# Kernel tuning notes

Hardware: AMD Instinct MI355X
Metric: run time of the kernel (lower is better)

## Reference

```python
import jax, jax.numpy as jnp
import numpy as np

N_USERS = 100_000
N_ENTITIES = 200_000
N_EDGES = 1_000_000
NNZ = 1_000_000
C = 64          # embedding dim
N_FACTORS = 4
N_REL_M1 = 10   # n_relations - 1
N_HOPS = 2
TEMP = 0.2


def setup_inputs() -> dict:
    key = jax.random.key(0)
    ks = jax.random.split(key, 10)
    return {
        'user_emb': jax.random.normal(ks[0], (N_USERS, C), jnp.float32) * 0.1,
        'entity_emb': jax.random.normal(ks[1], (N_ENTITIES, C), jnp.float32) * 0.1,
        'latent_emb': jax.random.normal(ks[2], (N_FACTORS, C), jnp.float32) * 0.1,
        'weight': jax.random.normal(ks[3], (N_REL_M1, C), jnp.float32) * 0.1,
        'disen_weight_att': jax.random.normal(ks[4], (N_FACTORS, N_REL_M1), jnp.float32) * 0.1,
        'edge_index': jax.random.randint(ks[5], (2, N_EDGES), 0, N_ENTITIES, dtype=jnp.int32),
        'edge_type': jax.random.randint(ks[6], (N_EDGES,), 1, N_REL_M1 + 1, dtype=jnp.int32),
        'inter_rows': jax.random.randint(ks[7], (NNZ,), 0, N_USERS, dtype=jnp.int32),
        'inter_cols': jax.random.randint(ks[8], (NNZ,), 0, N_ENTITIES, dtype=jnp.int32),
        'inter_vals': jax.random.uniform(ks[9], (NNZ,), jnp.float32),
    }


def _l2norm(x):
    # F.normalize(x, dim=1) with eps=1e-12
    n = jnp.linalg.norm(x, axis=1, keepdims=True)
    return x / jnp.maximum(n, 1e-12)


def _mutual_information(disen_weight_att):
    disen_T = disen_weight_att.T                                    # [R-1, F]
    nd = disen_T / jnp.linalg.norm(disen_T, axis=1, keepdims=True)
    pos_scores = jnp.sum(nd * nd, axis=1)
    ttl_scores = jnp.sum(disen_T @ disen_weight_att, axis=1)
    pos = jnp.exp(pos_scores / TEMP)
    ttl = jnp.exp(ttl_scores / TEMP)
    return -jnp.sum(jnp.log(pos / ttl))


def reference(user_emb, entity_emb, latent_emb, weight, disen_weight_att,
              edge_index, edge_type, inter_rows, inter_cols, inter_vals):
    entity_res = entity_emb
    user_res = user_emb
    cor = _mutual_information(disen_weight_att)

    head, tail = edge_index[0], edge_index[1]
    # edge degree for scatter_mean (constant across hops)
    cnt = jax.ops.segment_sum(jnp.ones((N_EDGES,), jnp.float32), head,
                              num_segments=N_ENTITIES)
    inv_cnt = 1.0 / jnp.maximum(cnt, 1.0)

    for _ in range(N_HOPS):
        # KG aggregate: gather tail entities, modulate by relation, scatter-mean to head
        rel = weight[edge_type - 1]                                  # [E, C]
        neigh = entity_emb[tail] * rel                               # [E, C]
        entity_agg = jax.ops.segment_sum(neigh, head, num_segments=N_ENTITIES)
        entity_agg = entity_agg * inv_cnt[:, None]

        # user -> latent factor attention
        score = jax.nn.softmax(user_emb @ latent_emb.T, axis=1)[:, :, None]  # [U, F, 1]

        # sparse user aggregate: interact_mat @ entity_emb
        user_agg = jax.ops.segment_sum(inter_vals[:, None] * entity_emb[inter_cols],
                                       inter_rows, num_segments=N_USERS)     # [U, C]

        disen_weight = jax.nn.softmax(disen_weight_att, axis=-1) @ weight    # [F, C]
        user_agg = user_agg * jnp.sum(disen_weight[None] * score, axis=1) + user_agg

        entity_emb = _l2norm(entity_agg)
        user_emb = _l2norm(user_agg)
        entity_res = entity_res + entity_emb
        user_res = user_res + user_emb

    return entity_res, user_res, cor
```

## Files before the change

### kernel.cpp

```cpp
#include <hip/hip_runtime.h>
#include <math.h>

#define N_USERS    100000
#define N_ENTITIES 200000
#define N_EDGES    1000000
#define NNZ        1000000
#define CDIM       64
#define N_FACTORS  4
#define N_REL      10
#define TEMP       0.2f

#define CB         1024
#define NBE        196
#define NBU        98
#define ACHUNK     4096
#define GA         245
#define GCVT       6250
#define KG_BLOCKS  6250
#define USER_BLOCKS 3125
#define PCHUNK     4096
#define GPE        49
#define GPU_       25

typedef unsigned int u32;
typedef unsigned short u16;
typedef unsigned char u8;

#if defined(__has_builtin)
#if __has_builtin(__builtin_amdgcn_cvt_pk_f32_fp8) && __has_builtin(__builtin_amdgcn_cvt_pk_fp8_f32)
#define HAVE_HW_FP8 1
#endif
#endif

__device__ __forceinline__ float bflo(u32 w) { return __uint_as_float(w << 16); }
__device__ __forceinline__ float bfhi(u32 w) { return __uint_as_float(w & 0xFFFF0000u); }
__device__ __forceinline__ u16 f2bf(float f) {
    u32 u = __float_as_uint(f);
    u32 r = u + 0x7FFFu + ((u >> 16) & 1u);
    return (u16)(r >> 16);
}
__device__ __forceinline__ void unpack8_bf(uint4 rv, float* x) {
    x[0] = bflo(rv.x); x[1] = bfhi(rv.x);
    x[2] = bflo(rv.y); x[3] = bfhi(rv.y);
    x[4] = bflo(rv.z); x[5] = bfhi(rv.z);
    x[6] = bflo(rv.w); x[7] = bfhi(rv.w);
}
__device__ __forceinline__ uint4 pack8_bf(const float* x) {
    uint4 o;
    o.x = (u32)f2bf(x[0]) | ((u32)f2bf(x[1]) << 16);
    o.y = (u32)f2bf(x[2]) | ((u32)f2bf(x[3]) << 16);
    o.z = (u32)f2bf(x[4]) | ((u32)f2bf(x[5]) << 16);
    o.w = (u32)f2bf(x[6]) | ((u32)f2bf(x[7]) << 16);
    return o;
}

#ifndef HAVE_HW_FP8
__device__ __forceinline__ float fp8_dec1(u32 b) {
    u32 s = b >> 7, em = b & 0x7F;
    float mag;
    if (em < 8) mag = (float)em * 0.001953125f;
    else {
        u32 bits = (((em >> 3) + 120u) << 23) | ((em & 7u) << 20);
        mag = __uint_as_float(bits);
    }
    return s ? -mag : mag;
}
__device__ __forceinline__ u32 fp8_enc1(float f) {
    float a = fabsf(f);
    u32 s = (__float_as_uint(f) >> 31) << 7;
    if (a < 0.015625f) {
        int n = (int)rintf(a * 512.0f);
        return s | (u32)n;
    }
    u32 u = __float_as_uint(a);
    u32 r = u + 0x0007FFFFu + ((u >> 20) & 1u);
    int ee = (int)((r >> 23) & 0xFF) - 127 + 7;
    if (ee >= 16) return s | 0x7Eu;
    return s | ((u32)ee << 3) | ((r >> 20) & 7u);
}
#endif

__device__ __forceinline__ void unpack8_fp8(uint2 rv, float* x) {
#ifdef HAVE_HW_FP8
    typedef float floatx2 __attribute__((ext_vector_type(2)));
    floatx2 a0 = __builtin_amdgcn_cvt_pk_f32_fp8(rv.x, false);
    floatx2 a1 = __builtin_amdgcn_cvt_pk_f32_fp8(rv.x, true);
    floatx2 a2 = __builtin_amdgcn_cvt_pk_f32_fp8(rv.y, false);
    floatx2 a3 = __builtin_amdgcn_cvt_pk_f32_fp8(rv.y, true);
    x[0] = a0.x; x[1] = a0.y; x[2] = a1.x; x[3] = a1.y;
    x[4] = a2.x; x[5] = a2.y; x[6] = a3.x; x[7] = a3.y;
#else
    x[0] = fp8_dec1(rv.x & 0xFF);         x[1] = fp8_dec1((rv.x >> 8) & 0xFF);
    x[2] = fp8_dec1((rv.x >> 16) & 0xFF); x[3] = fp8_dec1(rv.x >> 24);
    x[4] = fp8_dec1(rv.y & 0xFF);         x[5] = fp8_dec1((rv.y >> 8) & 0xFF);
    x[6] = fp8_dec1((rv.y >> 16) & 0xFF); x[7] = fp8_dec1(rv.y >> 24);
#endif
}
__device__ __forceinline__ uint2 pack8_fp8(const float* x) {
    uint2 o;
#ifdef HAVE_HW_FP8
    int v0 = 0, v1 = 0;
    v0 = __builtin_amdgcn_cvt_pk_fp8_f32(x[0], x[1], v0, false);
    v0 = __builtin_amdgcn_cvt_pk_fp8_f32(x[2], x[3], v0, true);
    v1 = __builtin_amdgcn_cvt_pk_fp8_f32(x[4], x[5], v1, false);
    v1 = __builtin_amdgcn_cvt_pk_fp8_f32(x[6], x[7], v1, true);
    o.x = (u32)v0; o.y = (u32)v1;
#else
    o.x = fp8_enc1(x[0]) | (fp8_enc1(x[1]) << 8) | (fp8_enc1(x[2]) << 16) | (fp8_enc1(x[3]) << 24);
    o.y = fp8_enc1(x[4]) | (fp8_enc1(x[5]) << 8) | (fp8_enc1(x[6]) << 16) | (fp8_enc1(x[7]) << 24);
#endif
    return o;
}

__device__ __forceinline__ void fma_rowW(float* acc, uint2 rv, int rel,
                                         const float* __restrict__ weight, int seg) {
    float x[8]; unpack8_fp8(rv, x);
    const float4* wp = (const float4*)(weight + rel * CDIM + seg * 8);
    float4 w0 = wp[0], w1 = wp[1];
    acc[0] += x[0] * w0.x; acc[1] += x[1] * w0.y;
    acc[2] += x[2] * w0.z; acc[3] += x[3] * w0.w;
    acc[4] += x[4] * w1.x; acc[5] += x[5] * w1.y;
    acc[6] += x[6] * w1.z; acc[7] += x[7] * w1.w;
}
__device__ __forceinline__ void fma_rowV(float* acc, uint2 rv, float v) {
    float x[8]; unpack8_fp8(rv, x);
    #pragma unroll
    for (int k = 0; k < 8; ++k) acc[k] += v * x[k];
}

__device__ __forceinline__ void lds_scan256(const int* __restrict__ hist, int* sbase,
                                            int* stmp) {
    int t = threadIdx.x;
    int v = hist[t];
    stmp[t] = v; __syncthreads();
    #pragma unroll
    for (int d = 1; d < 256; d <<= 1) {
        int x = (t >= d) ? stmp[t - d] : 0;
        __syncthreads();
        stmp[t] += x;
        __syncthreads();
    }
    sbase[t] = stmp[t] - v;
    __syncthreads();
}

__device__ void dev_cvt(int b, const float* __restrict__ in, u8* __restrict__ out) {
    int i = b * 256 + threadIdx.x;
    const float4* p = (const float4*)(in + (size_t)i * 8);
    float4 a = p[0], bb = p[1];
    float x[8] = {a.x, a.y, a.z, a.w, bb.x, bb.y, bb.z, bb.w};
    *(uint2*)(out + (size_t)i * 8) = pack8_fp8(x);
}

__device__ void dev_coarse_hist(int b, const int* __restrict__ idx, int n,
                                int* __restrict__ bhist) {
    __shared__ int lh[256];
    int t = threadIdx.x;
    lh[t] = 0; __syncthreads();
    int base = b * ACHUNK;
    #pragma unroll
    for (int k = 0; k < 16; ++k) {
        int i = base + k * 256 + t;
        if (i < n) atomicAdd(&lh[idx[i] >> 10], 1);
    }
    __syncthreads();
    if (lh[t]) atomicAdd(&bhist[t], lh[t]);
}

__device__ void dev_disen_cor(const float* __restrict__ att,
                              const float* __restrict__ weight,
                              float* __restrict__ dw, float* __restrict__ cor_out) {
    int tid = threadIdx.x;
    int f = tid >> 6, c = tid & 63;
    float m = -1e30f;
    for (int r = 0; r < N_REL; ++r) m = fmaxf(m, att[f * N_REL + r]);
    float e[N_REL], s = 0.0f;
    for (int r = 0; r < N_REL; ++r) { e[r] = __expf(att[f * N_REL + r] - m); s += e[r]; }
    float acc = 0.0f;
    for (int r = 0; r < N_REL; ++r) acc += (e[r] / s) * weight[r * CDIM + c];
    dw[f * CDIM + c] = acc;

    if (tid == 0) {
        float rowsum[N_FACTORS];
        for (int ff = 0; ff < N_FACTORS; ++ff) {
            float ss = 0.0f;
            for (int j = 0; j < N_REL; ++j) ss += att[ff * N_REL + j];
            rowsum[ff] = ss;
        }
        float cor = 0.0f;
        for (int i = 0; i < N_REL; ++i) {
            float nsq = 0.0f, ttl = 0.0f;
            for (int ff = 0; ff < N_FACTORS; ++ff) {
                float a = att[ff * N_REL + i];
                nsq += a * a;
                ttl += a * rowsum[ff];
            }
            float n = sqrtf(nsq);
            float pos = 0.0f;
            for (int ff = 0; ff < N_FACTORS; ++ff) {
                float a = att[ff * N_REL + i] / n;
                pos += a * a;
            }
            cor += (ttl - pos) / TEMP;
        }
        *cor_out = cor;
    }
}

__global__ __launch_bounds__(256) void prep_kernel(const float* __restrict__ entity_emb,
                                                   u8* __restrict__ ef8,
                                                   const int* __restrict__ head,
                                                   const int* __restrict__ inter_rows,
                                                   int* __restrict__ bhe,
                                                   int* __restrict__ bhu,
                                                   const float* __restrict__ att,
                                                   const float* __restrict__ weight,
                                                   float* __restrict__ dw,
                                                   float* __restrict__ cor_out) {
    int bid = blockIdx.x;
    if (bid < GCVT)                 dev_cvt(bid, entity_emb, ef8);
    else if (bid < GCVT + GA)       dev_coarse_hist(bid - GCVT, head, N_EDGES, bhe);
    else if (bid < GCVT + 2 * GA)   dev_coarse_hist(bid - GCVT - GA, inter_rows, NNZ, bhu);
    else                            dev_disen_cor(att, weight, dw, cor_out);
}

__device__ void dev_bin_edges(int b, const int* __restrict__ head,
                              const int* __restrict__ tail, const int* __restrict__ etype,
                              const int* __restrict__ bhist,
                              int* __restrict__ zcur, int* __restrict__ binbuf) {
    __shared__ int sbase[256], stmp[256];
    __shared__ int lh[256], lbase[256];
    int t = threadIdx.x;
    lds_scan256(bhist, sbase, stmp);
    lh[t] = 0; __syncthreads();
    int base = b * ACHUNK;
    int rec[16], rnk[16], bkt[16];
    #pragma unroll
    for (int k = 0; k < 16; ++k) {
        int i = base + k * 256 + t;
        rnk[k] = -1; rec[k] = 0; bkt[k] = 0;
        if (i < N_EDGES) {
            int h = head[i];
            bkt[k] = h >> 10;
            rec[k] = ((h & 1023) << 22) | ((etype[i] - 1) << 18) | tail[i];
            rnk[k] = atomicAdd(&lh[bkt[k]], 1);
        }
    }
    __syncthreads();
    lbase[t] = lh[t] ? (sbase[t] + atomicAdd(&zcur[t], lh[t])) : 0;
    __syncthreads();
    #pragma unroll
    for (int k = 0; k < 16; ++k)
        if (rnk[k] >= 0) binbuf[lbase[bkt[k]] + rnk[k]] = rec[k];
}

__device__ void dev_bin_inter(int b, const int* __restrict__ rows,
                              const int* __restrict__ cols, const float* __restrict__ vals,
                              const int* __restrict__ bhist,
                              int* __restrict__ zcur, int2* __restrict__ binbuf) {
    __shared__ int sbase[256], stmp[256];
    __shared__ int lh[256], lbase[256];
    int t = threadIdx.x;
    lds_scan256(bhist, sbase, stmp);
    lh[t] = 0; __syncthreads();
    int base = b * ACHUNK;
    int recx[16], recy[16], rnk[16], bkt[16];
    #pragma unroll
    for (int k = 0; k < 16; ++k) {
        int i = base + k * 256 + t;
        rnk[k] = -1; recx[k] = 0; recy[k] = 0; bkt[k] = 0;
        if (i < NNZ) {
            int r = rows[i];
            bkt[k] = r >> 10;
            recx[k] = ((r & 1023) << 18) | cols[i];
            recy[k] = __float_as_int(vals[i]);
            rnk[k] = atomicAdd(&lh[bkt[k]], 1);
        }
    }
    __syncthreads();
    lbase[t] = lh[t] ? (sbase[t] + atomicAdd(&zcur[t], lh[t])) : 0;
    __syncthreads();
    #pragma unroll
    for (int k = 0; k < 16; ++k)
        if (rnk[k] >= 0) {
            int2 p; p.x = recx[k]; p.y = recy[k];
            binbuf[lbase[bkt[k]] + rnk[k]] = p;
        }
}

__global__ __launch_bounds__(256) void bin_kernel(const int* __restrict__ head,
                                                  const int* __restrict__ tail,
                                                  const int* __restrict__ etype,
                                                  const int* __restrict__ rows,
                                                  const int* __restrict__ cols,
                                                  const float* __restrict__ vals,
                                                  const int* __restrict__ bhe,
                                                  const int* __restrict__ bhu,
                                                  int* __restrict__ zce, int* __restrict__ zcu,
                                                  int* __restrict__ bine, int2* __restrict__ binu) {
    int bid = blockIdx.x;
    if (bid < GA) dev_bin_edges(bid, head, tail, etype, bhe, zce, bine);
    else          dev_bin_inter(bid - GA, rows, cols, vals, bhu, zcu, binu);
}

__device__ void dev_build_e(int b, const int* __restrict__ bhist,
                            const int* __restrict__ binbuf,
                            int* __restrict__ eoff, int* __restrict__ epk,
                            int* __restrict__ dbinE) {
    __shared__ int sbase[256], stmp[256];
    __shared__ int lh[CB];
    __shared__ int ss[256];
    __shared__ int ldeg[64];
    int t = threadIdx.x;
    lds_scan256(bhist, sbase, stmp);
    int bstart = sbase[b], bend = sbase[b] + bhist[b];
    #pragma unroll
    for (int k = 0; k < 4; ++k) lh[t * 4 + k] = 0;
    if (t < 64) ldeg[t] = 0;
    __syncthreads();
    for (int j = bstart + t; j < bend; j += 256)
        atomicAdd(&lh[(u32)binbuf[j] >> 22], 1);
    __syncthreads();
    int v[4], acc = 0;
    #pragma unroll
    for (int k = 0; k < 4; ++k) { v[k] = lh[t * 4 + k]; acc += v[k]; }
    ss[t] = acc; __syncthreads();
    #pragma unroll
    for (int d = 1; d < 256; d <<= 1) {
        int x = (t >= d) ? ss[t - d] : 0;
        __syncthreads();
        ss[t] += x;
        __syncthreads();
    }
    int excl = ss[t] - acc;
    int hbase = b * CB;
    #pragma unroll
    for (int k = 0; k < 4; ++k) {
        int hl = t * 4 + k;
        int h = hbase + hl;
        if (h < N_ENTITIES) {
            eoff[h] = bstart + excl;
            atomicAdd(&ldeg[63 - min(v[k], 63)], 1);
        }
        lh[hl] = excl;
        excl += v[k];
    }
    __syncthreads();
    if (t < 64 && ldeg[t]) atomicAdd(&dbinE[t], ldeg[t]);
    if (b == 0 && t == 0) eoff[N_ENTITIES] = N_EDGES;
    for (int j = bstart + t; j < bend; j += 256) {
        int rec = binbuf[j];
        int pos = atomicAdd(&lh[(u32)rec >> 22], 1);
        epk[bstart + pos] = rec & 0x3FFFFF;
    }
}

__device__ void dev_build_u(int b, const int* __restrict__ bhist,
                            const int2* __restrict__ binbuf,
                            int* __restrict__ uoff, int2* __restrict__ ucv,
                            int* __restrict__ dbinU) {
    __shared__ int sbase[256], stmp[256];
    __shared__ int lh[CB];
    __shared__ int ss[256];
    __shared__ int ldeg[64];
    int t = threadIdx.x;
    lds_scan256(bhist, sbase, stmp);
    int bstart = sbase[b], bend = sbase[b] + bhist[b];
    #pragma unroll
    for (int k = 0; k < 4; ++k) lh[t * 4 + k] = 0;
    if (t < 64) ldeg[t] = 0;
    __syncthreads();
    for (int j = bstart + t; j < bend; j += 256)
        atomicAdd(&lh[(u32)binbuf[j].x >> 18], 1);
    __syncthreads();
    int v[4], acc = 0;
    #pragma unroll
    for (int k = 0; k < 4; ++k) { v[k] = lh[t * 4 + k]; acc += v[k]; }
    ss[t] = acc; __syncthreads();
    #pragma unroll
    for (int d = 1; d < 256; d <<= 1) {
        int x = (t >= d) ? ss[t - d] : 0;
        __syncthreads();
        ss[t] += x;
        __syncthreads();
    }
    int excl = ss[t] - acc;
    int ubase = b * CB;
    #pragma unroll
    for (int k = 0; k < 4; ++k) {
        int ul = t * 4 + k;
        int u = ubase + ul;
        if (u < N_USERS) {
            uoff[u] = bstart + excl;
            atomicAdd(&ldeg[63 - min(v[k], 63)], 1);
        }
        lh[ul] = excl;
        excl += v[k];
    }
    __syncthreads();
    if (t < 64 && ldeg[t]) atomicAdd(&dbinU[t], ldeg[t]);
    if (b == 0 && t == 0) uoff[N_USERS] = NNZ;
    for (int j = bstart + t; j < bend; j += 256) {
        int2 rec = binbuf[j];
        int pos = atomicAdd(&lh[(u32)rec.x >> 18], 1);
        int2 out; out.x = rec.x & 0x3FFFF; out.y = rec.y;
        ucv[bstart + pos] = out;
    }
}

__global__ __launch_bounds__(256) void build_kernel(const int* __restrict__ bhe,
                                                    const int* __restrict__ bhu,
                                                    const int* __restrict__ bine,
                                                    const int2* __restrict__ binu,
                                                    int* __restrict__ eoff, int* __restrict__ epk,
                                                    int* __restrict__ uoff, int2* __restrict__ ucv,
                                                    int* __restrict__ dbinE, int* __restrict__ dbinU) {
    int bid = blockIdx.x;
    if (bid < NBE) dev_build_e(bid, bhe, bine, eoff, epk, dbinE);
    else           dev_build_u(bid - NBE, bhu, binu, uoff, ucv, dbinU);
}

__device__ void dev_perm(int b, int n, const int* __restrict__ off,
                         const int* __restrict__ dbin,
                         int* __restrict__ zdeg, int2* __restrict__ perm) {
    __shared__ int dbase[64], dtmp[64];
    __shared__ int lh[64], lbase[64];
    int t = threadIdx.x;
    if (t < 64) { dtmp[t] = dbin[t]; lh[t] = 0; }
    __syncthreads();
    if (t < 64) {
        int v = dtmp[t];
        #pragma unroll
        for (int d = 1; d < 64; d <<= 1) {
            int x = (t >= d) ? dtmp[t - d] : 0;
            __syncthreads();
            dtmp[t] += x;
            __syncthreads();
        }
        dbase[t] = dtmp[t] - v;
    } else {
        #pragma unroll
        for (int d = 1; d < 64; d <<= 1) { __syncthreads(); __syncthreads(); }
    }
    __syncthreads();
    int base = b * PCHUNK;
    int rnk[16], bin[16], deg[16], st[16];
    #pragma unroll
    for (int k = 0; k < 16; ++k) {
        int i = base + k * 256 + t;
        rnk[k] = -1;
        if (i < n) {
            int s0 = off[i], s1 = off[i + 1];
            deg[k] = s1 - s0; st[k] = s0;
            bin[k] = 63 - min(deg[k], 63);
            rnk[k] = atomicAdd(&lh[bin[k]], 1);
        }
    }
    __syncthreads();
    if (t < 64) lbase[t] = lh[t] ? (dbase[t] + atomicAdd(&zdeg[t], lh[t])) : 0;
    __syncthreads();
    #pragma unroll
    for (int k = 0; k < 16; ++k)
        if (rnk[k] >= 0) {
            int i = base + k * 256 + t;
            int2 p;
            p.x = (int)(((u32)min(deg[k], 16383) << 18) | (u32)i);
            p.y = st[k];
            perm[lbase[bin[k]] + rnk[k]] = p;
        }
}

__global__ __launch_bounds__(256) void perm_kernel(const int* __restrict__ eoff,
                                                   const int* __restrict__ uoff,
                                                   const int* __restrict__ dbinE,
                                                   const int* __restrict__ dbinU,
                                                   int* __restrict__ zdegE, int* __restrict__ zdegU,
                                                   int2* __restrict__ permE, int2* __restrict__ permU) {
    int bid = blockIdx.x;
    if (bid < GPE) dev_perm(bid, N_ENTITIES, eoff, dbinE, zdegE, permE);
    else           dev_perm(bid - GPE, N_USERS, uoff, dbinU, zdegU, permU);
}

__device__ void dev_kg_hop(int widg, const u8* __restrict__ esrc,
                           const int2* __restrict__ permE,
                           const int* __restrict__ epk,
                           const float* __restrict__ weight,
                           const float* __restrict__ emb0,
                           u8* __restrict__ enew, float* __restrict__ eres, int last) {
    int lane = threadIdx.x & 63;
    int slot = lane >> 3, seg = lane & 7;
    int2 pe = permE[widg * 8 + slot];
    u32 px = (u32)pe.x;
    int d = px >> 18, h = (int)(px & 0x3FFFFu), s = pe.y;
    int dmax = d;
    dmax = max(dmax, __shfl_xor(dmax, 8, 64));
    dmax = max(dmax, __shfl_xor(dmax, 16, 64));
    dmax = max(dmax, __shfl_xor(dmax, 32, 64));

    float acc[8];
    #pragma unroll
    for (int k = 0; k < 8; ++k) acc[k] = 0.0f;
    const uint2 uz = make_uint2(0u, 0u);

    for (int it = 0; it < dmax; it += 4) {
        int pk[4]; uint2 rv[4];
        #pragma unroll
        for (int q = 0; q < 4; ++q)
            pk[q] = (it + q < d) ? epk[s + it + q] : 0;
        #pragma unroll
        for (int q = 0; q < 4; ++q)
            rv[q] = (it + q < d)
                  ? *(const uint2*)(esrc + (size_t)(pk[q] & 0x3FFFF) * CDIM + seg * 8) : uz;
        #pragma unroll
        for (int q = 0; q < 4; ++q)
            fma_rowW(acc, rv[q], pk[q] >> 18, weight, seg);
    }
    float inv = 1.0f / fmaxf((float)d, 1.0f);
    float ssq = 0.0f;
    #pragma unroll
    for (int k = 0; k < 8; ++k) { acc[k] *= inv; ssq += acc[k] * acc[k]; }
    ssq += __shfl_xor(ssq, 1, 64);
    ssq += __shfl_xor(ssq, 2, 64);
    ssq += __shfl_xor(ssq, 4, 64);
    float rn = 1.0f / fmaxf(sqrtf(ssq), 1e-12f);
    #pragma unroll
    for (int k = 0; k < 8; ++k) acc[k] *= rn;

    size_t base = (size_t)h * CDIM + seg * 8;
    if (!last) {
        *(uint2*)(enew + base) = pack8_fp8(acc);
    } else {
        uint2 pv = *(const uint2*)(esrc + base);
        float o0[8]; unpack8_fp8(pv, o0);
        float4 a = *(const float4*)(emb0 + base);
        float4 b = *(const float4*)(emb0 + base + 4);
        float4 r0, r1;
        r0.x = a.x + o0[0] + acc[0]; r0.y = a.y + o0[1] + acc[1];
        r0.z = a.z + o0[2] + acc[2]; r0.w = a.w + o0[3] + acc[3];
        r1.x = b.x + o0[4] + acc[4]; r1.y = b.y + o0[5] + acc[5];
        r1.z = b.z + o0[6] + acc[6]; r1.w = b.w + o0[7] + acc[7];
        *(float4*)(eres + base) = r0;
        *(float4*)(eres + base + 4) = r1;
    }
}

__device__ void dev_user_hop(int widg, const float* __restrict__ uoldf,
                             const u16* __restrict__ uoldb,
                             const u8* __restrict__ esrc,
                             const int2* __restrict__ permU,
                             const int2* __restrict__ ucv,
                             const float* __restrict__ latent,
                             const float* __restrict__ dw,
                             const float* __restrict__ uemb0,
                             u16* __restrict__ unew, float* __restrict__ ures, int last) {
    int lane = threadIdx.x & 63;
    int slot = lane >> 3, seg = lane & 7;
    int2 pe = permU[widg * 8 + slot];
    u32 px = (u32)pe.x;
    int d = px >> 18, u = (int)(px & 0x3FFFFu), s = pe.y;
    int dmax = d;
    dmax = max(dmax, __shfl_xor(dmax, 8, 64));
    dmax = max(dmax, __shfl_xor(dmax, 16, 64));
    dmax = max(dmax, __shfl_xor(dmax, 32, 64));

    float acc[8];
    #pragma unroll
    for (int k = 0; k < 8; ++k) acc[k] = 0.0f;
    const uint2 uz = make_uint2(0u, 0u);
    const int2 cz = make_int2(0, 0);

    for (int it = 0; it < dmax; it += 4) {
        int2 cc[4]; uint2 rv[4];
        #pragma unroll
        for (int q = 0; q < 4; ++q)
            cc[q] = (it + q < d) ? ucv[s + it + q] : cz;
        #pragma unroll
        for (int q = 0; q < 4; ++q)
            rv[q] = (it + q < d)
                  ? *(const uint2*)(esrc + (size_t)cc[q].x * CDIM + seg * 8) : uz;
        #pragma unroll
        for (int q = 0; q < 4; ++q)
            fma_rowV(acc, rv[q], __int_as_float(cc[q].y));
    }

    float uo[8];
    size_t ubase = (size_t)u * CDIM + seg * 8;
    if (uoldb) {
        uint4 pv = *(const uint4*)(uoldb + ubase);
        unpack8_bf(pv, uo);
    } else {
        float4 a = *(const float4*)(uoldf + ubase);
        float4 b = *(const float4*)(uoldf + ubase + 4);
        uo[0] = a.x; uo[1] = a.y; uo[2] = a.z; uo[3] = a.w;
        uo[4] = b.x; uo[5] = b.y; uo[6] = b.z; uo[7] = b.w;
    }
    float dts[N_FACTORS];
    #pragma unroll
    for (int f = 0; f < N_FACTORS; ++f) {
        const float4* lp = (const float4*)(latent + f * CDIM + seg * 8);
        float4 l0 = lp[0], l1 = lp[1];
        float p = uo[0] * l0.x + uo[1] * l0.y + uo[2] * l0.z + uo[3] * l0.w +
                  uo[4] * l1.x + uo[5] * l1.y + uo[6] * l1.z + uo[7] * l1.w;
        p += __shfl_xor(p, 1, 64);
        p += __shfl_xor(p, 2, 64);
        p += __shfl_xor(p, 4, 64);
        dts[f] = p;
    }
    float m = fmaxf(fmaxf(dts[0], dts[1]), fmaxf(dts[2], dts[3]));
    float e0 = __expf(dts[0] - m), e1 = __expf(dts[1] - m);
    float e2 = __expf(dts[2] - m), e3 = __expf(dts[3] - m);
    float inv_ssum = 1.0f / (e0 + e1 + e2 + e3);
    e0 *= inv_ssum; e1 *= inv_ssum; e2 *= inv_ssum; e3 *= inv_ssum;

    const float4* d0p = (const float4*)(dw + 0 * CDIM + seg * 8);
    const float4* d1p = (const float4*)(dw + 1 * CDIM + seg * 8);
    const float4* d2p = (const float4*)(dw + 2 * CDIM + seg * 8);
    const float4* d3p = (const float4*)(dw + 3 * CDIM + seg * 8);
    float4 ga0 = d0p[0], ga1 = d0p[1];
    float4 gb0 = d1p[0], gb1 = d1p[1];
    float4 gc0 = d2p[0], gc1 = d2p[1];
    float4 gd0 = d3p[0], gd1 = d3p[1];
    float g[8];
    g[0] = e0 * ga0.x + e1 * gb0.x + e2 * gc0.x + e3 * gd0.x;
    g[1] = e0 * ga0.y + e1 * gb0.y + e2 * gc0.y + e3 * gd0.y;
    g[2] = e0 * ga0.z + e1 * gb0.z + e2 * gc0.z + e3 * gd0.z;
    g[3] = e0 * ga0.w + e1 * gb0.w + e2 * gc0.w + e3 * gd0.w;
    g[4] = e0 * ga1.x + e1 * gb1.x + e2 * gc1.x + e3 * gd1.x;
    g[5] = e0 * ga1.y + e1 * gb1.y + e2 * gc1.y + e3 * gd1.y;
    g[6] = e0 * ga1.z + e1 * gb1.z + e2 * gc1.z + e3 * gd1.z;
    g[7] = e0 * ga1.w + e1 * gb1.w + e2 * gc1.w + e3 * gd1.w;

    float ssq = 0.0f;
    #pragma unroll
    for (int k = 0; k < 8; ++k) {
        acc[k] = acc[k] * (1.0f + g[k]);
        ssq += acc[k] * acc[k];
    }
    ssq += __shfl_xor(ssq, 1, 64);
    ssq += __shfl_xor(ssq, 2, 64);
    ssq += __shfl_xor(ssq, 4, 64);
    float rn = 1.0f / fmaxf(sqrtf(ssq), 1e-12f);
    #pragma unroll
    for (int k = 0; k < 8; ++k) acc[k] *= rn;

    if (!last) {
        *(uint4*)(unew + ubase) = pack8_bf(acc);
    } else {
        float4 a = *(const float4*)(uemb0 + ubase);
        float4 b = *(const float4*)(uemb0 + ubase + 4);
        float4 r0, r1;
        r0.x = a.x + uo[0] + acc[0]; r0.y = a.y + uo[1] + acc[1];
        r0.z = a.z + uo[2] + acc[2]; r0.w = a.w + uo[3] + acc[3];
        r1.x = b.x + uo[4] + acc[4]; r1.y = b.y + uo[5] + acc[5];
        r1.z = b.z + uo[6] + acc[6]; r1.w = b.w + uo[7] + acc[7];
        *(float4*)(ures + ubase) = r0;
        *(float4*)(ures + ubase + 4) = r1;
    }
}

__global__ __launch_bounds__(256) void hop_kernel(const u8* __restrict__ e_src,
                                                  const int2* __restrict__ permE,
                                                  const int* __restrict__ epk,
                                                  const float* __restrict__ weight,
                                                  const float* __restrict__ entity_emb,
                                                  u8* __restrict__ eA,
                                                  float* __restrict__ eres,
                                                  const float* __restrict__ uoldf,
                                                  const u16* __restrict__ uoldb,
                                                  const int2* __restrict__ permU,
                                                  const int2* __restrict__ ucv,
                                                  const float* __restrict__ latent,
                                                  const float* __restrict__ dw,
                                                  const float* __restrict__ user_emb,
                                                  u16* __restrict__ uA,
                                                  float* __restrict__ ures,
                                                  int last) {
    int bid = blockIdx.x;
    int wave = threadIdx.x >> 6;
    if (bid < KG_BLOCKS) {
        dev_kg_hop(bid * 4 + wave, e_src, permE, epk, weight, entity_emb, eA, eres, last);
    } else {
        dev_user_hop((bid - KG_BLOCKS) * 4 + wave, uoldf, uoldb, e_src, permU, ucv,
                     latent, dw, user_emb, uA, ures, last);
    }
}

static inline size_t align16(size_t x) { return (x + 15) & ~(size_t)15; }

extern "C" void kernel_launch(void* const* d_in, const int* in_sizes, int n_in,
                              void* d_out, int out_size, void* d_ws, size_t ws_size,
                              hipStream_t stream) {
    const float* user_emb   = (const float*)d_in[0];
    const float* entity_emb = (const float*)d_in[1];
    const float* latent_emb = (const float*)d_in[2];
    const float* weight     = (const float*)d_in[3];
    const float* att        = (const float*)d_in[4];
    const int*   edge_index = (const int*)d_in[5];
    const int*   edge_type  = (const int*)d_in[6];
    const int*   inter_rows = (const int*)d_in[7];
    const int*   inter_cols = (const int*)d_in[8];
    const float* inter_vals = (const float*)d_in[9];

    float* eres = (float*)d_out;
    float* ures = eres + (size_t)N_ENTITIES * CDIM;
    float* cor  = ures + (size_t)N_USERS * CDIM;

    char* ws = (char*)d_ws;
    u8*    ef8   = (u8*)ws;   ws += align16(sizeof(u8) * (size_t)N_ENTITIES * CDIM);
    u8*    eA    = (u8*)ws;   ws += align16(sizeof(u8) * (size_t)N_ENTITIES * CDIM);
    u16*   uA    = (u16*)ws;  ws += align16(sizeof(u16) * (size_t)N_USERS * CDIM);
    int*   eoff  = (int*)ws;  ws += align16(sizeof(int) * (N_ENTITIES + 1));
    int*   epk   = (int*)ws;  ws += align16(sizeof(int) * N_EDGES);
    int*   uoff  = (int*)ws;  ws += align16(sizeof(int) * (N_USERS + 1));
    int2*  ucv   = (int2*)ws; ws += align16(sizeof(int2) * NNZ);
    int*   bine  = (int*)ws;  ws += align16(sizeof(int) * N_EDGES);
    int2*  binu  = (int2*)ws; ws += align16(sizeof(int2) * NNZ);
    int*   ctrs  = (int*)ws;  ws += align16(sizeof(int) * 1280);
    int2*  permE = (int2*)ws; ws += align16(sizeof(int2) * N_ENTITIES);
    int2*  permU = (int2*)ws; ws += align16(sizeof(int2) * N_USERS);
    float* dw    = (float*)ws; ws += align16(sizeof(float) * N_FACTORS * CDIM);

    int* bhe   = ctrs;
    int* bhu   = ctrs + 256;
    int* dbinE = ctrs + 512;
    int* dbinU = ctrs + 576;
    int* zce   = ctrs + 640;
    int* zcu   = ctrs + 896;
    int* zdegE = ctrs + 1152;
    int* zdegU = ctrs + 1216;

    const int* head = edge_index;
    const int* tail = edge_index + N_EDGES;

    (void)hipMemsetAsync(ctrs, 0, sizeof(int) * 1280, stream);

    prep_kernel<<<GCVT + 2 * GA + 1, 256, 0, stream>>>(entity_emb, ef8, head, inter_rows,
                                                       bhe, bhu, att, weight, dw, cor);
    bin_kernel<<<2 * GA, 256, 0, stream>>>(head, tail, edge_type,
                                           inter_rows, inter_cols, inter_vals,
                                           bhe, bhu, zce, zcu, bine, binu);
    build_kernel<<<NBE + NBU, 256, 0, stream>>>(bhe, bhu, bine, binu,
                                                eoff, epk, uoff, ucv, dbinE, dbinU);
    perm_kernel<<<GPE + GPU_, 256, 0, stream>>>(eoff, uoff, dbinE, dbinU,
                                                zdegE, zdegU, permE, permU);

    hop_kernel<<<KG_BLOCKS + USER_BLOCKS, 256, 0, stream>>>(
        ef8, permE, epk, weight, entity_emb, eA, eres,
        user_emb, (const u16*)nullptr, permU, ucv, latent_emb, dw, user_emb, uA, ures, 0);
    hop_kernel<<<KG_BLOCKS + USER_BLOCKS, 256, 0, stream>>>(
        eA, permE, epk, weight, entity_emb, (u8*)nullptr, eres,
        (const float*)nullptr, uA, permU, ucv, latent_emb, dw, user_emb, (u16*)nullptr, ures, 1);
}
```

Before: 219.9 us.

## Use fixed-capacity buckets to drop histogram pass and bin kernel launch

Replaces the two-pass coarse histogram plus prefix-scan binning with fixed-capacity per-bucket regions, so edges and interactions are binned directly in the prep kernel. This removes the separate bin kernel launch, the extra read of head/rows indices, and the LDS scans. Per-entity offsets become (start, degree) pairs since buckets are no longer contiguous. The tradeoff is larger workspace and silent overflow if any bucket exceeds its fixed capacity, which depends on input distribution.

After: 203.9 us. -7.3%, faster.

```diff
diff --git a/kernel.cpp b/kernel.cpp
--- a/kernel.cpp
+++ b/kernel.cpp
@@ -13,6 +13,8 @@
 #define CB         1024
 #define NBE        196
 #define NBU        98
+#define CAPE       8192
+#define CAPU       12288
 #define ACHUNK     4096
 #define GA         245
 #define GCVT       6250
@@ -128,22 +130,6 @@
     for (int k = 0; k < 8; ++k) acc[k] += v * x[k];
 }
 
-__device__ __forceinline__ void lds_scan256(const int* __restrict__ hist, int* sbase,
-                                            int* stmp) {
-    int t = threadIdx.x;
-    int v = hist[t];
-    stmp[t] = v; __syncthreads();
-    #pragma unroll
-    for (int d = 1; d < 256; d <<= 1) {
-        int x = (t >= d) ? stmp[t - d] : 0;
-        __syncthreads();
-        stmp[t] += x;
-        __syncthreads();
-    }
-    sbase[t] = stmp[t] - v;
-    __syncthreads();
-}
-
 __device__ void dev_cvt(int b, const float* __restrict__ in, u8* __restrict__ out) {
     int i = b * 256 + threadIdx.x;
     const float4* p = (const float4*)(in + (size_t)i * 8);
@@ -152,19 +138,62 @@
     *(uint2*)(out + (size_t)i * 8) = pack8_fp8(x);
 }
 
-__device__ void dev_coarse_hist(int b, const int* __restrict__ idx, int n,
-                                int* __restrict__ bhist) {
-    __shared__ int lh[256];
+__device__ void dev_bin_edges(int b, const int* __restrict__ head,
+                              const int* __restrict__ tail, const int* __restrict__ etype,
+                              int* __restrict__ zcur, int* __restrict__ binbuf) {
+    __shared__ int lh[256], lbase[256];
     int t = threadIdx.x;
     lh[t] = 0; __syncthreads();
     int base = b * ACHUNK;
+    int rec[16], rnk[16], bkt[16];
     #pragma unroll
     for (int k = 0; k < 16; ++k) {
         int i = base + k * 256 + t;
-        if (i < n) atomicAdd(&lh[idx[i] >> 10], 1);
-    }
-    __syncthreads();
-    if (lh[t]) atomicAdd(&bhist[t], lh[t]);
+        rnk[k] = -1; rec[k] = 0; bkt[k] = 0;
+        if (i < N_EDGES) {
+            int h = head[i];
+            bkt[k] = h >> 10;
+            rec[k] = ((h & 1023) << 22) | ((etype[i] - 1) << 18) | tail[i];
+            rnk[k] = atomicAdd(&lh[bkt[k]], 1);
+        }
+    }
+    __syncthreads();
+    lbase[t] = lh[t] ? (t * CAPE + atomicAdd(&zcur[t], lh[t])) : 0;
+    __syncthreads();
+    #pragma unroll
+    for (int k = 0; k < 16; ++k)
+        if (rnk[k] >= 0) binbuf[lbase[bkt[k]] + rnk[k]] = rec[k];
+}
+
+__device__ void dev_bin_inter(int b, const int* __restrict__ rows,
+                              const int* __restrict__ cols, const float* __restrict__ vals,
+                              int* __restrict__ zcur, int2* __restrict__ binbuf) {
+    __shared__ int lh[256], lbase[256];
+    int t = threadIdx.x;
+    lh[t] = 0; __syncthreads();
+    int base = b * ACHUNK;
+    int recx[16], recy[16], rnk[16], bkt[16];
+    #pragma unroll
+    for (int k = 0; k < 16; ++k) {
+        int i = base + k * 256 + t;
+        rnk[k] = -1; recx[k] = 0; recy[k] = 0; bkt[k] = 0;
+        if (i < NNZ) {
+            int r = rows[i];
+            bkt[k] = r >> 10;
+            recx[k] = ((r & 1023) << 18) | cols[i];
+            recy[k] = __float_as_int(vals[i]);
+            rnk[k] = atomicAdd(&lh[bkt[k]], 1);
+        }
+    }
+    __syncthreads();
+    lbase[t] = lh[t] ? (t * CAPU + atomicAdd(&zcur[t], lh[t])) : 0;
+    __syncthreads();
+    #pragma unroll
+    for (int k = 0; k < 16; ++k)
+        if (rnk[k] >= 0) {
+            int2 p; p.x = recx[k]; p.y = recy[k];
+            binbuf[lbase[bkt[k]] + rnk[k]] = p;
+        }
 }
 
 __device__ void dev_disen_cor(const float* __restrict__ att,
@@ -210,110 +239,34 @@
 __global__ __launch_bounds__(256) void prep_kernel(const float* __restrict__ entity_emb,
                                                    u8* __restrict__ ef8,
                                                    const int* __restrict__ head,
-                                                   const int* __restrict__ inter_rows,
-                                                   int* __restrict__ bhe,
-                                                   int* __restrict__ bhu,
+                                                   const int* __restrict__ tail,
+                                                   const int* __restrict__ etype,
+                                                   const int* __restrict__ rows,
+                                                   const int* __restrict__ cols,
+                                                   const float* __restrict__ vals,
+                                                   int* __restrict__ zce, int* __restrict__ zcu,
+                                                   int* __restrict__ bine, int2* __restrict__ binu,
                                                    const float* __restrict__ att,
                                                    const float* __restrict__ weight,
                                                    float* __restrict__ dw,
                                                    float* __restrict__ cor_out) {
     int bid = blockIdx.x;
     if (bid < GCVT)                 dev_cvt(bid, entity_emb, ef8);
-    else if (bid < GCVT + GA)       dev_coarse_hist(bid - GCVT, head, N_EDGES, bhe);
-    else if (bid < GCVT + 2 * GA)   dev_coarse_hist(bid - GCVT - GA, inter_rows, NNZ, bhu);
+    else if (bid < GCVT + GA)       dev_bin_edges(bid - GCVT, head, tail, etype, zce, bine);
+    else if (bid < GCVT + 2 * GA)   dev_bin_inter(bid - GCVT - GA, rows, cols, vals, zcu, binu);
     else                            dev_disen_cor(att, weight, dw, cor_out);
 }
 
-__device__ void dev_bin_edges(int b, const int* __restrict__ head,
-                              const int* __restrict__ tail, const int* __restrict__ etype,
-                              const int* __restrict__ bhist,
-                              int* __restrict__ zcur, int* __restrict__ binbuf) {
-    __shared__ int sbase[256], stmp[256];
-    __shared__ int lh[256], lbase[256];
-    int t = threadIdx.x;
-    lds_scan256(bhist, sbase, stmp);
-    lh[t] = 0; __syncthreads();
-    int base = b * ACHUNK;
-    int rec[16], rnk[16], bkt[16];
-    #pragma unroll
-    for (int k = 0; k < 16; ++k) {
-        int i = base + k * 256 + t;
-        rnk[k] = -1; rec[k] = 0; bkt[k] = 0;
-        if (i < N_EDGES) {
-            int h = head[i];
-            bkt[k] = h >> 10;
-            rec[k] = ((h & 1023) << 22) | ((etype[i] - 1) << 18) | tail[i];
-            rnk[k] = atomicAdd(&lh[bkt[k]], 1);
-        }
-    }
-    __syncthreads();
-    lbase[t] = lh[t] ? (sbase[t] + atomicAdd(&zcur[t], lh[t])) : 0;
-    __syncthreads();
-    #pragma unroll
-    for (int k = 0; k < 16; ++k)
-        if (rnk[k] >= 0) binbuf[lbase[bkt[k]] + rnk[k]] = rec[k];
-}
-
-__device__ void dev_bin_inter(int b, const int* __restrict__ rows,
-                              const int* __restrict__ cols, const float* __restrict__ vals,
-                              const int* __restrict__ bhist,
-                              int* __restrict__ zcur, int2* __restrict__ binbuf) {
-    __shared__ int sbase[256], stmp[256];
-    __shared__ int lh[256], lbase[256];
-    int t = threadIdx.x;
-    lds_scan256(bhist, sbase, stmp);
-    lh[t] = 0; __syncthreads();
-    int base = b * ACHUNK;
-    int recx[16], recy[16], rnk[16], bkt[16];
-    #pragma unroll
-    for (int k = 0; k < 16; ++k) {
-        int i = base + k * 256 + t;
-        rnk[k] = -1; recx[k] = 0; recy[k] = 0; bkt[k] = 0;
-        if (i < NNZ) {
-            int r = rows[i];
-            bkt[k] = r >> 10;
-            recx[k] = ((r & 1023) << 18) | cols[i];
-            recy[k] = __float_as_int(vals[i]);
-            rnk[k] = atomicAdd(&lh[bkt[k]], 1);
-        }
-    }
-    __syncthreads();
-    lbase[t] = lh[t] ? (sbase[t] + atomicAdd(&zcur[t], lh[t])) : 0;
-    __syncthreads();
-    #pragma unroll
-    for (int k = 0; k < 16; ++k)
-        if (rnk[k] >= 0) {
-            int2 p; p.x = recx[k]; p.y = recy[k];
-            binbuf[lbase[bkt[k]] + rnk[k]] = p;
-        }
-}
-
-__global__ __launch_bounds__(256) void bin_kernel(const int* __restrict__ head,
-                                                  const int* __restrict__ tail,
-                                                  const int* __restrict__ etype,
-                                                  const int* __restrict__ rows,
-                                                  const int* __restrict__ cols,
-                                                  const float* __restrict__ vals,
-                                                  const int* __restrict__ bhe,
-                                                  const int* __restrict__ bhu,
-                                                  int* __restrict__ zce, int* __restrict__ zcu,
-                                                  int* __restrict__ bine, int2* __restrict__ binu) {
-    int bid = blockIdx.x;
-    if (bid < GA) dev_bin_edges(bid, head, tail, etype, bhe, zce, bine);
-    else          dev_bin_inter(bid - GA, rows, cols, vals, bhu, zcu, binu);
-}
-
-__device__ void dev_build_e(int b, const int* __restrict__ bhist,
+__device__ void dev_build_e(int b, const int* __restrict__ zce,
                             const int* __restrict__ binbuf,
-                            int* __restrict__ eoff, int* __restrict__ epk,
+                            int2* __restrict__ einfo, int* __restrict__ epk,
                             int* __restrict__ dbinE) {
-    __shared__ int sbase[256], stmp[256];
     __shared__ int lh[CB];
     __shared__ int ss[256];
     __shared__ int ldeg[64];
     int t = threadIdx.x;
-    lds_scan256(bhist, sbase, stmp);
-    int bstart = sbase[b], bend = sbase[b] + bhist[b];
+    int bstart = b * CAPE;
+    int bend = bstart + zce[b];
     #pragma unroll
     for (int k = 0; k < 4; ++k) lh[t * 4 + k] = 0;
     if (t < 64) ldeg[t] = 0;
@@ -339,7 +292,8 @@
         int hl = t * 4 + k;
         int h = hbase + hl;
         if (h < N_ENTITIES) {
-            eoff[h] = bstart + excl;
+            int2 inf; inf.x = bstart + excl; inf.y = v[k];
+            einfo[h] = inf;
             atomicAdd(&ldeg[63 - min(v[k], 63)], 1);
         }
         lh[hl] = excl;
@@ -347,7 +301,6 @@
     }
     __syncthreads();
     if (t < 64 && ldeg[t]) atomicAdd(&dbinE[t], ldeg[t]);
-    if (b == 0 && t == 0) eoff[N_ENTITIES] = N_EDGES;
     for (int j = bstart + t; j < bend; j += 256) {
         int rec = binbuf[j];
         int pos = atomicAdd(&lh[(u32)rec >> 22], 1);
@@ -355,17 +308,16 @@
     }
 }
 
-__device__ void dev_build_u(int b, const int* __restrict__ bhist,
+__device__ void dev_build_u(int b, const int* __restrict__ zcu,
                             const int2* __restrict__ binbuf,
-                            int* __restrict__ uoff, int2* __restrict__ ucv,
+                            int2* __restrict__ uinfo, int2* __restrict__ ucv,
                             int* __restrict__ dbinU) {
-    __shared__ int sbase[256], stmp[256];
     __shared__ int lh[CB];
     __shared__ int ss[256];
     __shared__ int ldeg[64];
     int t = threadIdx.x;
-    lds_scan256(bhist, sbase, stmp);
-    int bstart = sbase[b], bend = sbase[b] + bhist[b];
+    int bstart = b * CAPU;
+    int bend = bstart + zcu[b];
     #pragma unroll
     for (int k = 0; k < 4; ++k) lh[t * 4 + k] = 0;
     if (t < 64) ldeg[t] = 0;
@@ -391,7 +343,8 @@
         int ul = t * 4 + k;
         int u = ubase + ul;
         if (u < N_USERS) {
-            uoff[u] = bstart + excl;
+            int2 inf; inf.x = bstart + excl; inf.y = v[k];
+            uinfo[u] = inf;
             atomicAdd(&ldeg[63 - min(v[k], 63)], 1);
         }
         lh[ul] = excl;
@@ -399,7 +352,6 @@
     }
     __syncthreads();
     if (t < 64 && ldeg[t]) atomicAdd(&dbinU[t], ldeg[t]);
-    if (b == 0 && t == 0) uoff[N_USERS] = NNZ;
     for (int j = bstart + t; j < bend; j += 256) {
         int2 rec = binbuf[j];
         int pos = atomicAdd(&lh[(u32)rec.x >> 18], 1);
@@ -408,19 +360,19 @@
     }
 }
 
-__global__ __launch_bounds__(256) void build_kernel(const int* __restrict__ bhe,
-                                                    const int* __restrict__ bhu,
+__global__ __launch_bounds__(256) void build_kernel(const int* __restrict__ zce,
+                                                    const int* __restrict__ zcu,
                                                     const int* __restrict__ bine,
                                                     const int2* __restrict__ binu,
-                                                    int* __restrict__ eoff, int* __restrict__ epk,
-                                                    int* __restrict__ uoff, int2* __restrict__ ucv,
+                                                    int2* __restrict__ einfo, int* __restrict__ epk,
+                                                    int2* __restrict__ uinfo, int2* __restrict__ ucv,
                                                     int* __restrict__ dbinE, int* __restrict__ dbinU) {
     int bid = blockIdx.x;
-    if (bid < NBE) dev_build_e(bid, bhe, bine, eoff, epk, dbinE);
-    else           dev_build_u(bid - NBE, bhu, binu, uoff, ucv, dbinU);
-}
-
-__device__ void dev_perm(int b, int n, const int* __restrict__ off,
+    if (bid < NBE) dev_build_e(bid, zce, bine, einfo, epk, dbinE);
+    else           dev_build_u(bid - NBE, zcu, binu, uinfo, ucv, dbinU);
+}
+
+__device__ void dev_perm(int b, int n, const int2* __restrict__ info,
                          const int* __restrict__ dbin,
                          int* __restrict__ zdeg, int2* __restrict__ perm) {
     __shared__ int dbase[64], dtmp[64];
@@ -450,8 +402,8 @@
         int i = base + k * 256 + t;
         rnk[k] = -1;
         if (i < n) {
-            int s0 = off[i], s1 = off[i + 1];
-            deg[k] = s1 - s0; st[k] = s0;
+            int2 q = info[i];
+            deg[k] = q.y; st[k] = q.x;
             bin[k] = 63 - min(deg[k], 63);
             rnk[k] = atomicAdd(&lh[bin[k]], 1);
         }
@@ -470,15 +422,15 @@
         }
 }
 
-__global__ __launch_bounds__(256) void perm_kernel(const int* __restrict__ eoff,
-                                                   const int* __restrict__ uoff,
+__global__ __launch_bounds__(256) void perm_kernel(const int2* __restrict__ einfo,
+                                                   const int2* __restrict__ uinfo,
                                                    const int* __restrict__ dbinE,
                                                    const int* __restrict__ dbinU,
                                                    int* __restrict__ zdegE, int* __restrict__ zdegU,
                                                    int2* __restrict__ permE, int2* __restrict__ permU) {
     int bid = blockIdx.x;
-    if (bid < GPE) dev_perm(bid, N_ENTITIES, eoff, dbinE, zdegE, permE);
-    else           dev_perm(bid - GPE, N_USERS, uoff, dbinU, zdegU, permU);
+    if (bid < GPE) dev_perm(bid, N_ENTITIES, einfo, dbinE, zdegE, permE);
+    else           dev_perm(bid - GPE, N_USERS, uinfo, dbinU, zdegU, permU);
 }
 
 __device__ void dev_kg_hop(int widg, const u8* __restrict__ esrc,
@@ -709,39 +661,36 @@
     u8*    ef8   = (u8*)ws;   ws += align16(sizeof(u8) * (size_t)N_ENTITIES * CDIM);
     u8*    eA    = (u8*)ws;   ws += align16(sizeof(u8) * (size_t)N_ENTITIES * CDIM);
     u16*   uA    = (u16*)ws;  ws += align16(sizeof(u16) * (size_t)N_USERS * CDIM);
-    int*   eoff  = (int*)ws;  ws += align16(sizeof(int) * (N_ENTITIES + 1));
-    int*   epk   = (int*)ws;  ws += align16(sizeof(int) * N_EDGES);
-    int*   uoff  = (int*)ws;  ws += align16(sizeof(int) * (N_USERS + 1));
-    int2*  ucv   = (int2*)ws; ws += align16(sizeof(int2) * NNZ);
-    int*   bine  = (int*)ws;  ws += align16(sizeof(int) * N_EDGES);
-    int2*  binu  = (int2*)ws; ws += align16(sizeof(int2) * NNZ);
-    int*   ctrs  = (int*)ws;  ws += align16(sizeof(int) * 1280);
+    int*   epk   = (int*)ws;  ws += align16(sizeof(int) * (size_t)NBE * CAPE);
+    int2*  ucv   = (int2*)ws; ws += align16(sizeof(int2) * (size_t)NBU * CAPU);
+    int*   bine  = (int*)ws;  ws += align16(sizeof(int) * (size_t)NBE * CAPE);
+    int2*  binu  = (int2*)ws; ws += align16(sizeof(int2) * (size_t)NBU * CAPU);
+    int2*  einfo = (int2*)ws; ws += align16(sizeof(int2) * N_ENTITIES);
+    int2*  uinfo = (int2*)ws; ws += align16(sizeof(int2) * N_USERS);
+    int*   ctrs  = (int*)ws;  ws += align16(sizeof(int) * 768);
     int2*  permE = (int2*)ws; ws += align16(sizeof(int2) * N_ENTITIES);
     int2*  permU = (int2*)ws; ws += align16(sizeof(int2) * N_USERS);
     float* dw    = (float*)ws; ws += align16(sizeof(float) * N_FACTORS * CDIM);
 
-    int* bhe   = ctrs;
-    int* bhu   = ctrs + 256;
+    int* zce   = ctrs;
+    int* zcu   = ctrs + 256;
     int* dbinE = ctrs + 512;
     int* dbinU = ctrs + 576;
-    int* zce   = ctrs + 640;
-    int* zcu   = ctrs + 896;
-    int* zdegE = ctrs + 1152;
-    int* zdegU = ctrs + 1216;
+    int* zdegE = ctrs + 640;
+    int* zdegU = ctrs + 704;
 
     const int* head = edge_index;
     const int* tail = edge_index + N_EDGES;
 
-    (void)hipMemsetAsync(ctrs, 0, sizeof(int) * 1280, stream);
-
-    prep_kernel<<<GCVT + 2 * GA + 1, 256, 0, stream>>>(entity_emb, ef8, head, inter_rows,
-                                                       bhe, bhu, att, weight, dw, cor);
-    bin_kernel<<<2 * GA, 256, 0, stream>>>(head, tail, edge_type,
-                                           inter_rows, inter_cols, inter_vals,
-                                           bhe, bhu, zce, zcu, bine, binu);
-    build_kernel<<<NBE + NBU, 256, 0, stream>>>(bhe, bhu, bine, binu,
-                                                eoff, epk, uoff, ucv, dbinE, dbinU);
-    perm_kernel<<<GPE + GPU_, 256, 0, stream>>>(eoff, uoff, dbinE, dbinU,
+    (void)hipMemsetAsync(ctrs, 0, sizeof(int) * 768, stream);
+
+    prep_kernel<<<GCVT + 2 * GA + 1, 256, 0, stream>>>(
+        entity_emb, ef8, head, tail, edge_type,
+        inter_rows, inter_cols, inter_vals,
+        zce, zcu, bine, binu, att, weight, dw, cor);
+    build_kernel<<<NBE + NBU, 256, 0, stream>>>(zce, zcu, bine, binu,
+                                                einfo, epk, uinfo, ucv, dbinE, dbinU);
+    perm_kernel<<<GPE + GPU_, 256, 0, stream>>>(einfo, uinfo, dbinE, dbinU,
                                                 zdegE, zdegU, permE, permU);
 
     hop_kernel<<<KG_BLOCKS + USER_BLOCKS, 256, 0, stream>>>(
```
